# Kernel optimization log

Measured on AMD Instinct MI355X. Metric: run time of the kernel, lower is better.

The kernel has to match this reference:

```python
import jax, jax.numpy as jnp
import numpy as np


def setup_inputs() -> dict:
    key = jax.random.key(0)
    k1, k2, k3 = jax.random.split(key, 3)
    B, T, C, F = 32, 4096, 256, 256
    scale = 1.0 / np.sqrt(2 * C)  # glorot-ish fan-in scaling for kernel_size=2
    return {
        "x": jax.random.normal(k1, (B, T, C), dtype=jnp.float32),
        "Wv": jax.random.normal(k2, (2, C, F), dtype=jnp.float32) * scale,
        "bv": jnp.zeros((F,), dtype=jnp.float32),
        "Wg": jax.random.normal(k3, (2, C, F), dtype=jnp.float32) * scale,
        "bg": jnp.zeros((F,), dtype=jnp.float32),
        "dilation": 4,
    }


def _causal_dilated_k2(x, W, b, d):
    # Causal Conv1D, kernel_size=2, dilation d: y[t] = x[t-d] @ W[0] + x[t] @ W[1] + b
    T = x.shape[1]
    x_prev = jnp.pad(x, ((0, 0), (d, 0), (0, 0)))[:, :T]  # left-pad with zeros
    return (jnp.einsum("btc,cf->btf", x_prev, W[0])
            + jnp.einsum("btc,cf->btf", x, W[1]) + b)


def reference(x, Wv, bv, Wg, bg, dilation):
    value = jnp.tanh(_causal_dilated_k2(x, Wv, bv, dilation))
    gate = jax.nn.sigmoid(_causal_dilated_k2(x, Wg, bg, dilation))
    activations = value * gate
    # gate_merge = Concatenate (channel axis by default in Keras for 3D tensors)
    return jnp.concatenate([activations, x], axis=-1)
```

## Files before the change

kernel.cpp:

```cpp
#include <hip/hip_runtime.h>
#include <hip/hip_bf16.h>
#include <cstdint>

#define B_    32
#define T_    4096
#define C_    256
#define BM    64
#define DMAX  16
#define NROWS (BM + DMAX)

typedef __attribute__((ext_vector_type(8))) short bf16x8;
typedef __attribute__((ext_vector_type(4))) float f32x4;
typedef __attribute__((ext_vector_type(4))) short s16x4;

static __device__ __forceinline__ short f2bf(float f) {
  __hip_bfloat16 h = __float2bfloat16(f);
  union { __hip_bfloat16 h; short s; } u; u.h = h;
  return u.s;
}

static __device__ __forceinline__ float rcp_(float x) {
  return __builtin_amdgcn_rcpf(x);
}

__global__ void prep_weights(const float* __restrict__ Wv, const float* __restrict__ Wg,
                             const float* __restrict__ bv, const float* __restrict__ bg,
                             short* __restrict__ wimg, float* __restrict__ bcat) {
  int id = blockIdx.x * 256 + threadIdx.x;
  int kk = id & 31;
  int np = (id >> 5) & 255;
  int ks = (id >> 13) & 15;
  int nb = id >> 17;
  int k = ks * 32 + kk, tap = k >> 8, kr = k & 255;
  int sel = np >> 7;
  int f = nb * 128 + (np & 127);
  const float* W = sel ? Wg : Wv;
  wimg[id] = f2bf(W[((size_t)tap * 256 + kr) * 256 + f]);
  if (id < 512) bcat[id] = (id < 256) ? bv[id] : bg[id - 256];
}

__global__ __launch_bounds__(256, 4) void snail_main(
    const float* __restrict__ x, const short* __restrict__ wimg,
    const float* __restrict__ bcat, const int* __restrict__ dptr,
    float* __restrict__ out) {
  __shared__ __align__(16) short lx[NROWS * C_];

  const int d = *dptr;
  const int bid = blockIdx.x;
  const int swz = (bid & 7) * 512 + (bid >> 3);
  const int nb = swz & 1;
  const int t0 = ((swz >> 1) & 63) * BM;
  const int b  = swz >> 7;

  const int tid  = threadIdx.x;
  const int lane = tid & 63;
  const int w    = tid >> 6;
  const int row15 = lane & 15;
  const int qw    = lane >> 4;

  const float* xb = x + (size_t)b * T_ * C_;
  float* ob = out + (size_t)b * T_ * 512;

  for (int i = tid; i < d * 64; i += 256) {
    int r = i >> 6, c4 = i & 63;
    int t = t0 - d + r;
    f32x4 v = (f32x4){0.f, 0.f, 0.f, 0.f};
    if (t >= 0) v = *(const f32x4*)(xb + (size_t)t * C_ + c4 * 4);
    s16x4 s;
    s.x = f2bf(v.x); s.y = f2bf(v.y); s.z = f2bf(v.z); s.w = f2bf(v.w);
    int byte = (r * 512 + c4 * 8) ^ ((r & 7) << 4);
    *(s16x4*)((char*)lx + byte) = s;
  }
#pragma unroll 4
  for (int ii = 0; ii < 16; ++ii) {
    int i = ii * 256 + tid;
    int rr = i >> 6, c4 = i & 63;
    int t = t0 + rr, r = rr + d;
    f32x4 v = *(const f32x4*)(xb + (size_t)t * C_ + c4 * 4);
    if ((c4 >> 5) == nb)
      __builtin_nontemporal_store(v, (f32x4*)(ob + (size_t)t * 512 + C_ + c4 * 4));
    s16x4 s;
    s.x = f2bf(v.x); s.y = f2bf(v.y); s.z = f2bf(v.z); s.w = f2bf(v.w);
    int byte = (r * 512 + c4 * 8) ^ ((r & 7) << 4);
    *(s16x4*)((char*)lx + byte) = s;
  }
  __syncthreads();

  f32x4 accv[4][2], accg[4][2];
#pragma unroll
  for (int mi = 0; mi < 4; ++mi)
#pragma unroll
    for (int ni = 0; ni < 2; ++ni) {
      accv[mi][ni] = (f32x4){0.f, 0.f, 0.f, 0.f};
      accg[mi][ni] = (f32x4){0.f, 0.f, 0.f, 0.f};
    }

  const short* wl = wimg + (size_t)nb * 131072 + (w * 32 + row15) * 32 + qw * 8;

#define LOADW(D0, D1, D2, D3, KS) do {                                  \
    const short* wk_ = wl + (KS) * 8192;                                \
    D0 = *(const bf16x8*)(wk_);                                         \
    D1 = *(const bf16x8*)(wk_ + 512);                                   \
    D2 = *(const bf16x8*)(wk_ + 4096);                                  \
    D3 = *(const bf16x8*)(wk_ + 4608);                                  \
  } while (0)

#define STEP(B0, B1, G0, G1, KS) do {                                   \
    bf16x8 af[4];                                                       \
    const int rofs_ = ((KS) >= 8) ? d : 0;                              \
    const int cb_ = ((KS) & 7) * 64 + qw * 16;                          \
    _Pragma("unroll")                                                   \
    for (int mi = 0; mi < 4; ++mi) {                                    \
      int r_ = 16 * mi + row15 + rofs_;                                 \
      af[mi] = *(const bf16x8*)((const char*)lx +                       \
               ((r_ * 512 + cb_) ^ ((r_ & 7) << 4)));                   \
    }                                                                   \
    _Pragma("unroll")                                                   \
    for (int mi = 0; mi < 4; ++mi) {                                    \
      accv[mi][0] = __builtin_amdgcn_mfma_f32_16x16x32_bf16(B0, af[mi], accv[mi][0], 0, 0, 0); \
      accv[mi][1] = __builtin_amdgcn_mfma_f32_16x16x32_bf16(B1, af[mi], accv[mi][1], 0, 0, 0); \
      accg[mi][0] = __builtin_amdgcn_mfma_f32_16x16x32_bf16(G0, af[mi], accg[mi][0], 0, 0, 0); \
      accg[mi][1] = __builtin_amdgcn_mfma_f32_16x16x32_bf16(G1, af[mi], accg[mi][1], 0, 0, 0); \
    }                                                                   \
  } while (0)

  bf16x8 a0, a1, a2, a3, b0, b1, b2, b3;
  LOADW(a0, a1, a2, a3, 0);
#pragma unroll 1
  for (int ks2 = 0; ks2 < 8; ++ks2) {
    LOADW(b0, b1, b2, b3, 2 * ks2 + 1);
    STEP(a0, a1, a2, a3, 2 * ks2);
    if (ks2 < 7) LOADW(a0, a1, a2, a3, 2 * ks2 + 2);
    STEP(b0, b1, b2, b3, 2 * ks2 + 1);
  }
#undef LOADW
#undef STEP

#pragma unroll
  for (int ni = 0; ni < 2; ++ni) {
    int f0 = nb * 128 + w * 32 + 16 * ni + qw * 4;
    f32x4 bv4 = *(const f32x4*)(bcat + f0);
    f32x4 bg4 = *(const f32x4*)(bcat + 256 + f0);
#pragma unroll
    for (int mi = 0; mi < 4; ++mi) {
      int t = t0 + 16 * mi + row15;
      f32x4 v = accv[mi][ni], g = accg[mi][ni];
      f32x4 res;
#pragma unroll
      for (int j = 0; j < 4; ++j) {
        float vv = v[j] + bv4[j], gg = g[j] + bg4[j];
        float th = 1.f - 2.f * rcp_(__expf(2.f * vv) + 1.f);
        float sg = rcp_(1.f + __expf(-gg));
        res[j] = th * sg;
      }
      __builtin_nontemporal_store(res, (f32x4*)(ob + (size_t)t * 512 + f0));
    }
  }
}

extern "C" void kernel_launch(void* const* d_in, const int* in_sizes, int n_in,
                              void* d_out, int out_size, void* d_ws, size_t ws_size,
                              hipStream_t stream) {
  const float* x  = (const float*)d_in[0];
  const float* Wv = (const float*)d_in[1];
  const float* bv = (const float*)d_in[2];
  const float* Wg = (const float*)d_in[3];
  const float* bg = (const float*)d_in[4];
  const int* dil  = (const int*)d_in[5];
  float* out = (float*)d_out;

  short* wimg = (short*)d_ws;
  float* bcat = (float*)((char*)d_ws + 16 * 32768);

  prep_weights<<<1024, 256, 0, stream>>>(Wv, Wg, bv, bg, wimg, bcat);
  snail_main<<<B_ * (T_ / BM) * 2, 256, 0, stream>>>(x, wimg, bcat, dil, out);
}
```

Measured before the change: 121.8 us.

## Pipeline x staging into LDS by column chunks, overlapping loads with MFMA

```diff
diff --git a/kernel.cpp b/kernel.cpp
--- a/kernel.cpp
+++ b/kernel.cpp
@@ -61,30 +61,40 @@
   const float* xb = x + (size_t)b * T_ * C_;
   float* ob = out + (size_t)b * T_ * 512;
 
-  for (int i = tid; i < d * 64; i += 256) {
-    int r = i >> 6, c4 = i & 63;
-    int t = t0 - d + r;
-    f32x4 v = (f32x4){0.f, 0.f, 0.f, 0.f};
-    if (t >= 0) v = *(const f32x4*)(xb + (size_t)t * C_ + c4 * 4);
-    s16x4 s;
-    s.x = f2bf(v.x); s.y = f2bf(v.y); s.z = f2bf(v.z); s.w = f2bf(v.w);
-    int byte = (r * 512 + c4 * 8) ^ ((r & 7) << 4);
-    *(s16x4*)((char*)lx + byte) = s;
-  }
-#pragma unroll 4
-  for (int ii = 0; ii < 16; ++ii) {
-    int i = ii * 256 + tid;
-    int rr = i >> 6, c4 = i & 63;
-    int t = t0 + rr, r = rr + d;
-    f32x4 v = *(const f32x4*)(xb + (size_t)t * C_ + c4 * 4);
-    if ((c4 >> 5) == nb)
-      __builtin_nontemporal_store(v, (f32x4*)(ob + (size_t)t * 512 + C_ + c4 * 4));
-    s16x4 s;
-    s.x = f2bf(v.x); s.y = f2bf(v.y); s.z = f2bf(v.z); s.w = f2bf(v.w);
-    int byte = (r * 512 + c4 * 8) ^ ((r & 7) << 4);
-    *(s16x4*)((char*)lx + byte) = s;
-  }
-  __syncthreads();
+  const int nrows = BM + d;
+
+  f32x4 sreg[3];
+
+#define STAGE_LOAD(CB) do {                                             \
+    _Pragma("unroll")                                                   \
+    for (int j = 0; j < 3; ++j) {                                       \
+      int idx = j * 256 + tid;                                          \
+      int r_ = idx >> 3, c4_ = (CB) * 8 + (idx & 7);                    \
+      int t_ = t0 - d + r_;                                             \
+      sreg[j] = (f32x4){0.f, 0.f, 0.f, 0.f};                            \
+      if (r_ < nrows && t_ >= 0)                                        \
+        sreg[j] = *(const f32x4*)(xb + (size_t)t_ * C_ + c4_ * 4);      \
+    }                                                                   \
+  } while (0)
+
+#define STAGE_WRITE(CB) do {                                            \
+    _Pragma("unroll")                                                   \
+    for (int j = 0; j < 3; ++j) {                                       \
+      int idx = j * 256 + tid;                                          \
+      int r_ = idx >> 3, c4_ = (CB) * 8 + (idx & 7);                    \
+      int t_ = t0 - d + r_;                                             \
+      if (r_ < nrows) {                                                 \
+        if (r_ >= d && ((CB) >> 2) == nb)                               \
+          __builtin_nontemporal_store(sreg[j],                          \
+              (f32x4*)(ob + (size_t)t_ * 512 + C_ + c4_ * 4));          \
+        s16x4 s_;                                                       \
+        s_.x = f2bf(sreg[j].x); s_.y = f2bf(sreg[j].y);                 \
+        s_.z = f2bf(sreg[j].z); s_.w = f2bf(sreg[j].w);                 \
+        int byte_ = (r_ * 512 + c4_ * 8) ^ ((r_ & 7) << 4);             \
+        *(s16x4*)((char*)lx + byte_) = s_;                              \
+      }                                                                 \
+    }                                                                   \
+  } while (0)
 
   f32x4 accv[4][2], accg[4][2];
 #pragma unroll
@@ -97,15 +107,12 @@
 
   const short* wl = wimg + (size_t)nb * 131072 + (w * 32 + row15) * 32 + qw * 8;
 
-#define LOADW(D0, D1, D2, D3, KS) do {                                  \
+#define STEP(KS) do {                                                   \
     const short* wk_ = wl + (KS) * 8192;                                \
-    D0 = *(const bf16x8*)(wk_);                                         \
-    D1 = *(const bf16x8*)(wk_ + 512);                                   \
-    D2 = *(const bf16x8*)(wk_ + 4096);                                  \
-    D3 = *(const bf16x8*)(wk_ + 4608);                                  \
-  } while (0)
-
-#define STEP(B0, B1, G0, G1, KS) do {                                   \
+    bf16x8 w0 = *(const bf16x8*)(wk_);                                  \
+    bf16x8 w1 = *(const bf16x8*)(wk_ + 512);                            \
+    bf16x8 w2 = *(const bf16x8*)(wk_ + 4096);                           \
+    bf16x8 w3 = *(const bf16x8*)(wk_ + 4608);                           \
     bf16x8 af[4];                                                       \
     const int rofs_ = ((KS) >= 8) ? d : 0;                              \
     const int cb_ = ((KS) & 7) * 64 + qw * 16;                          \
@@ -117,24 +124,28 @@
     }                                                                   \
     _Pragma("unroll")                                                   \
     for (int mi = 0; mi < 4; ++mi) {                                    \
-      accv[mi][0] = __builtin_amdgcn_mfma_f32_16x16x32_bf16(B0, af[mi], accv[mi][0], 0, 0, 0); \
-      accv[mi][1] = __builtin_amdgcn_mfma_f32_16x16x32_bf16(B1, af[mi], accv[mi][1], 0, 0, 0); \
-      accg[mi][0] = __builtin_amdgcn_mfma_f32_16x16x32_bf16(G0, af[mi], accg[mi][0], 0, 0, 0); \
-      accg[mi][1] = __builtin_amdgcn_mfma_f32_16x16x32_bf16(G1, af[mi], accg[mi][1], 0, 0, 0); \
+      accv[mi][0] = __builtin_amdgcn_mfma_f32_16x16x32_bf16(w0, af[mi], accv[mi][0], 0, 0, 0); \
+      accv[mi][1] = __builtin_amdgcn_mfma_f32_16x16x32_bf16(w1, af[mi], accv[mi][1], 0, 0, 0); \
+      accg[mi][0] = __builtin_amdgcn_mfma_f32_16x16x32_bf16(w2, af[mi], accg[mi][0], 0, 0, 0); \
+      accg[mi][1] = __builtin_amdgcn_mfma_f32_16x16x32_bf16(w3, af[mi], accg[mi][1], 0, 0, 0); \
     }                                                                   \
   } while (0)
 
-  bf16x8 a0, a1, a2, a3, b0, b1, b2, b3;
-  LOADW(a0, a1, a2, a3, 0);
+  STAGE_LOAD(0);
+  STAGE_WRITE(0);
+  __syncthreads();
+
 #pragma unroll 1
-  for (int ks2 = 0; ks2 < 8; ++ks2) {
-    LOADW(b0, b1, b2, b3, 2 * ks2 + 1);
-    STEP(a0, a1, a2, a3, 2 * ks2);
-    if (ks2 < 7) LOADW(a0, a1, a2, a3, 2 * ks2 + 2);
-    STEP(b0, b1, b2, b3, 2 * ks2 + 1);
+  for (int c = 0; c < 8; ++c) {
+    if (c < 7) STAGE_LOAD(c + 1);
+    STEP(c);
+    STEP(c + 8);
+    if (c < 7) STAGE_WRITE(c + 1);
+    __syncthreads();
   }
-#undef LOADW
 #undef STEP
+#undef STAGE_LOAD
+#undef STAGE_WRITE
 
 #pragma unroll
   for (int ni = 0; ni < 2; ++ni) {
```

Result: slower. 130.9 us (+7.4%).
